# Optimization experiments

Measured on AMD Instinct MI355X. Metric: run time of the kernel, lower is better.

## Reference

```python
import jax, jax.numpy as jnp
import numpy as np

N_HEAD = 16
N_EMBD = 1024
HEAD_DIM = N_EMBD // N_HEAD
ROPE_BASE = 10000.0


def _rope_tables(T, dim):
    inv_freq = 1.0 / (ROPE_BASE ** (jnp.arange(0, dim, 2, dtype=jnp.float32) / dim))
    t = jnp.arange(T, dtype=jnp.float32)
    freqs = jnp.einsum('i,j->ij', t, inv_freq)          # [T, dim/2]
    emb = jnp.concatenate((freqs, freqs), axis=-1)       # [T, dim]
    return jnp.cos(emb), jnp.sin(emb)


def _rotate_half(x):
    x1, x2 = jnp.split(x, 2, axis=-1)
    return jnp.concatenate((-x2, x1), axis=-1)


def setup_inputs() -> dict:
    key = jax.random.key(0)
    k_x, k_wa, k_ba, k_wp, k_bp = jax.random.split(key, 5)
    B, T, C = 2, 2048, N_EMBD
    x = jax.random.normal(k_x, (B, T, C), dtype=jnp.float32)
    # torch Linear weights: [out, in]
    W_attn = jax.random.normal(k_wa, (3 * C, C), dtype=jnp.float32) * (1.0 / np.sqrt(C))
    b_attn = jax.random.normal(k_ba, (3 * C,), dtype=jnp.float32) * 0.01
    W_proj = jax.random.normal(k_wp, (C, C), dtype=jnp.float32) * (1.0 / np.sqrt(C))
    b_proj = jax.random.normal(k_bp, (C,), dtype=jnp.float32) * 0.01
    return {"x": x, "W_attn": W_attn, "b_attn": b_attn, "W_proj": W_proj, "b_proj": b_proj}


def reference(x, W_attn, b_attn, W_proj, b_proj):
    B, T, C = x.shape
    H, D = N_HEAD, HEAD_DIM
    qkv = jnp.einsum('btc,oc->bto', x, W_attn) + b_attn   # [B,T,3C]
    q, k, v = jnp.split(qkv, 3, axis=2)
    # [B,T,C] -> [B,H,T,D]
    q = q.reshape(B, T, H, D).transpose(0, 2, 1, 3)
    k = k.reshape(B, T, H, D).transpose(0, 2, 1, 3)
    v = v.reshape(B, T, H, D).transpose(0, 2, 1, 3)
    cos, sin = _rope_tables(T, D)                          # [T,D]
    q = q * cos + _rotate_half(q) * sin
    k = k * cos + _rotate_half(k) * sin
    att = jnp.einsum('bhqd,bhkd->bhqk', q, k) * (1.0 / np.sqrt(D))
    causal = jnp.tril(jnp.ones((T, T), dtype=bool))
    att = jnp.where(causal, att, -jnp.inf)
    att = jax.nn.softmax(att, axis=-1)
    y = jnp.einsum('bhqk,bhkd->bhqd', att, v)              # [B,H,T,D]
    y = y.transpose(0, 2, 1, 3).reshape(B, T, C)
    y = jnp.einsum('btc,oc->bto', y, W_proj) + b_proj
    return y
```

## Files before the change

### kernel.cpp

```cpp
#include <hip/hip_runtime.h>


typedef unsigned short u16;
typedef u16 u16x4 __attribute__((ext_vector_type(4)));
typedef u16 u16x8 __attribute__((ext_vector_type(8)));
typedef short s16x4 __attribute__((ext_vector_type(4)));
typedef short s16x8 __attribute__((ext_vector_type(8)));
typedef float f32x4 __attribute__((ext_vector_type(4)));

#define T_SEQ 2048
#define C_EMB 1024
#define NH 16
#define HD 64

#define MFMA16(a, b, c) __builtin_amdgcn_mfma_f32_16x16x32_bf16(a, b, c, 0, 0, 0)

__device__ __forceinline__ f32x4 MFMA16K16(s16x4 a, s16x4 b, f32x4 c) {
#if __has_builtin(__builtin_amdgcn_mfma_f32_16x16x16bf16_1k)
    return __builtin_amdgcn_mfma_f32_16x16x16bf16_1k(a, b, c, 0, 0, 0);
#else
    asm("v_mfma_f32_16x16x16_bf16 %0, %1, %2, %0" : "+v"(c) : "v"(a), "v"(b));
    return c;
#endif
}

__device__ __forceinline__ u16 f2bf(float f) {
    union { float f; unsigned int i; } x; x.f = f;
    unsigned int r = x.i + 0x7fffu + ((x.i >> 16) & 1u);
    return (u16)(r >> 16);
}
__device__ __forceinline__ u16x4 pack4(f32x4 v) {
    u16x4 o;
#pragma unroll
    for (int j = 0; j < 4; ++j) o[j] = f2bf(v[j]);
    return o;
}
__device__ __forceinline__ s16x4 pack4cvt_s(f32x4 v) {
    union { s16x4 h; unsigned int w[2]; } u;
    asm("v_cvt_pk_bf16_f32 %0, %1, %2" : "=v"(u.w[0]) : "v"(v[0]), "v"(v[1]));
    asm("v_cvt_pk_bf16_f32 %0, %1, %2" : "=v"(u.w[1]) : "v"(v[2]), "v"(v[3]));
    return u.h;
}
__device__ __forceinline__ void gload16(const void* g, void* l) {
    __builtin_amdgcn_global_load_lds(
        (const __attribute__((address_space(1))) unsigned int*)g,
        (__attribute__((address_space(3))) unsigned int*)l, 16, 0, 0);
}

__global__ __launch_bounds__(256) void prep_k(const float* __restrict__ x, const float* __restrict__ Wa,
                                              const float* __restrict__ Wp,
                                              u16* __restrict__ xb, u16* __restrict__ Wab,
                                              u16* __restrict__ Wpb, float2* __restrict__ tab) {
    int bid = blockIdx.x, tid = threadIdx.x;
    if (bid < 4096) {
        const float* src;
        u16* dst;
        int i;
        if (bid < 2048)      { src = x;  dst = xb;  i = bid * 256 + tid; }
        else if (bid < 3584) { src = Wa; dst = Wab; i = (bid - 2048) * 256 + tid; }
        else                 { src = Wp; dst = Wpb; i = (bid - 3584) * 256 + tid; }
        f32x4 a = ((const f32x4*)src)[i * 2];
        f32x4 b = ((const f32x4*)src)[i * 2 + 1];
        u16x8 o;
#pragma unroll
        for (int j = 0; j < 4; ++j) o[j] = f2bf(a[j]);
#pragma unroll
        for (int j = 0; j < 4; ++j) o[4 + j] = f2bf(b[j]);
        ((u16x8*)dst)[i] = o;
    } else {
        int idx = (bid - 4096) * 256 + tid;
        int t = idx >> 5, j = idx & 31;
        float inv = __builtin_exp2f(-0.41524101186092f * (float)j);
        float s_, c_;
        sincosf((float)t * inv, &s_, &c_);
        tab[idx] = make_float2(c_, s_);
    }
}

__global__ __launch_bounds__(256) void qkv_rope_k(const u16* __restrict__ xb, const u16* __restrict__ Wab,
                                                  const float* __restrict__ bias,
                                                  const float2* __restrict__ tab,
                                                  u16* __restrict__ qb, u16* __restrict__ kb,
                                                  u16* __restrict__ vt) {
    __shared__ u16 smem[24576];
    u16* As = smem;
    u16* Bs = smem + 12288;
    int tid = threadIdx.x;
    int n0 = blockIdx.x * 128, m0 = blockIdx.y * 128;
    int w = tid >> 6, lane = tid & 63, lr = lane & 15, quad = lane >> 4;
    int wr = w >> 1, wc = w & 1;
    f32x4 acc[4][4] = {};
    int srow = tid >> 2;
    int swc8 = (((tid & 3) ^ (srow & 3)) << 3);
    int soff = tid * 8;
    int rc8 = ((quad ^ (lr & 3)) << 3);

#define QKV_STAGE(bufi, kc) do {                                                   \
        int _b = (bufi) * 4096;                                                    \
        gload16(xb  + (size_t)(m0 + srow) * C_EMB + (kc) + swc8,      &As[_b + soff]);        \
        gload16(xb  + (size_t)(m0 + 64 + srow) * C_EMB + (kc) + swc8, &As[_b + 2048 + soff]); \
        gload16(Wab + (size_t)(n0 + srow) * C_EMB + (kc) + swc8,      &Bs[_b + soff]);        \
        gload16(Wab + (size_t)(n0 + 64 + srow) * C_EMB + (kc) + swc8, &Bs[_b + 2048 + soff]); \
    } while (0)

    QKV_STAGE(0, 0);
    QKV_STAGE(1, 32);
    int cur = 0;
    for (int kt = 0; kt < 32; ++kt) {
        if (kt < 30) {
            int nb = cur + 2; if (nb >= 3) nb -= 3;
            QKV_STAGE(nb, (kt + 2) * 32);
            asm volatile("s_waitcnt vmcnt(8)" ::: "memory");
        } else if (kt == 30) {
            asm volatile("s_waitcnt vmcnt(4)" ::: "memory");
        } else {
            asm volatile("s_waitcnt vmcnt(0)" ::: "memory");
        }
        __builtin_amdgcn_s_barrier();
        asm volatile("" ::: "memory");
        int cb = cur * 4096;
        s16x8 af[4], bf[4];
#pragma unroll
        for (int i = 0; i < 4; ++i)
            af[i] = *(const s16x8*)&As[cb + (wr * 64 + i * 16 + lr) * 32 + rc8];
#pragma unroll
        for (int j = 0; j < 4; ++j)
            bf[j] = *(const s16x8*)&Bs[cb + (wc * 64 + j * 16 + lr) * 32 + rc8];
#pragma unroll
        for (int i = 0; i < 4; ++i)
#pragma unroll
            for (int j = 0; j < 4; ++j) acc[i][j] = MFMA16(af[i], bf[j], acc[i][j]);
        asm volatile("" ::: "memory");
        __builtin_amdgcn_s_barrier();
        cur = cur + 1; if (cur >= 3) cur -= 3;
    }
#undef QKV_STAGE

    int sec = n0 >> 10;
    float bv[4];
#pragma unroll
    for (int j = 0; j < 4; ++j) bv[j] = bias[n0 + wc * 64 + j * 16 + lr];

    int h0 = (n0 & 1023) >> 6;
    int b = m0 >> 11, tbase = m0 & 2047;
    if (sec == 2) {
        u16* Ct = smem;
#pragma unroll
        for (int i = 0; i < 4; ++i)
#pragma unroll
            for (int j = 0; j < 4; ++j) {
                f32x4 vv;
#pragma unroll
                for (int r = 0; r < 4; ++r) vv[r] = acc[i][j][r] + bv[j];
                int d = wc * 64 + j * 16 + lr;
                int m4 = wr * 64 + i * 16 + quad * 4;
                *(u16x4*)&Ct[d * 136 + m4] = pack4(vv);
            }
        __syncthreads();
        size_t hb = (size_t)(b * NH);
#pragma unroll
        for (int p = 0; p < 8; ++p) {
            int idx = p * 256 + tid;
            int d = idx >> 4, mc = (idx & 15) << 3;
            s16x8 vdat = *(const s16x8*)&Ct[d * 136 + mc];
            int h = h0 + (d >> 6), dd = d & 63;
            *(s16x8*)(vt + ((hb + h) * HD + dd) * T_SEQ + tbase + mc) = vdat;
        }
    } else {
        u16* dst = (sec == 0) ? qb : kb;
        float qs = (sec == 0) ? 0.18033688011112043f : 1.0f;
        u16* Ct = smem;
        __syncthreads();
#pragma unroll
        for (int i = 0; i < 4; ++i)
#pragma unroll
            for (int r = 0; r < 4; ++r) {
                int mrow = wr * 64 + i * 16 + quad * 4 + r;
                int t = (m0 + mrow) & 2047;
#pragma unroll
                for (int j = 0; j < 2; ++j) {
                    int d1 = j * 16 + lr;
                    float2 cs = tab[t * 32 + d1];
                    float v1 = acc[i][j][r] + bv[j];
                    float v2 = acc[i][j + 2][r] + bv[j + 2];
                    int n1 = wc * 64 + j * 16 + lr;
                    Ct[mrow * 136 + n1]      = f2bf((v1 * cs.x - v2 * cs.y) * qs);
                    Ct[mrow * 136 + n1 + 32] = f2bf((v2 * cs.x + v1 * cs.y) * qs);
                }
            }
        __syncthreads();
#pragma unroll
        for (int p = 0; p < 8; ++p) {
            int idx = p * 256 + tid;
            int mrow = idx >> 4, c = idx & 15;
            s16x8 vdat = *(const s16x8*)&Ct[mrow * 136 + c * 8];
            int h = h0 + (c >> 3), dd = (c & 7) << 3;
            *(s16x8*)(dst + ((size_t)(b * NH + h) * T_SEQ + tbase + mrow) * HD + dd) = vdat;
        }
    }
}

__global__ __launch_bounds__(256, 4) void flash_k(const u16* __restrict__ qb, const u16* __restrict__ kb,
                                                  const u16* __restrict__ vt, u16* __restrict__ yab) {
    __shared__ u16 Ks[2][64 * 72];
    __shared__ u16 Vs[2][64 * 72];
    int tid = threadIdx.x;
    int bx = blockIdx.x, by = blockIdx.y;
    int bh = by;
    int w = tid >> 6, lane = tid & 63, lr = lane & 15, quad = lane >> 4;
    const u16* qh = qb + (size_t)bh * T_SEQ * HD;
    const u16* kh = kb + (size_t)bh * T_SEQ * HD;
    const u16* vh = vt + (size_t)bh * HD * T_SEQ;
    int srow = tid >> 3, sc8 = (tid & 7) << 3;
    int b = bh >> 4, hh = bh & 15;

    for (int ph = 0; ph < 2; ++ph) {
        int qt = ph ? (31 - bx) : bx;
        int q0 = qt * 64;
        int rbase = q0 + w * 16;

        s16x8 aq[2];
#pragma unroll
        for (int ks = 0; ks < 2; ++ks)
            aq[ks] = *(const s16x8*)(qh + (size_t)(rbase + lr) * HD + ks * 32 + quad * 8);

        float m_i = -1e30f;
        f32x4 l4 = {0.f, 0.f, 0.f, 0.f};
        f32x4 oacc[4] = {};

        int ktmax = qt;
        {
            s16x8 ka = *(const s16x8*)(kh + (size_t)srow * HD + sc8);
            s16x8 kb2 = *(const s16x8*)(kh + (size_t)(srow + 32) * HD + sc8);
            s16x8 va = *(const s16x8*)(vh + (size_t)srow * T_SEQ + sc8);
            s16x8 vb = *(const s16x8*)(vh + (size_t)(srow + 32) * T_SEQ + sc8);
            *(s16x8*)&Ks[0][srow * 72 + sc8] = ka;
            *(s16x8*)&Ks[0][(srow + 32) * 72 + sc8] = kb2;
            *(s16x8*)&Vs[0][srow * 72 + sc8] = va;
            *(s16x8*)&Vs[0][(srow + 32) * 72 + sc8] = vb;
        }
        __syncthreads();

        for (int kt = 0; kt <= ktmax; ++kt) {
            int cur = kt & 1;
            int k0 = kt * 64;
            bool pf = kt < ktmax;
            s16x8 kr0, kr1, vr0, vr1;
            if (pf) {
                int kn = k0 + 64;
                kr0 = *(const s16x8*)(kh + (size_t)(kn + srow) * HD + sc8);
                kr1 = *(const s16x8*)(kh + (size_t)(kn + srow + 32) * HD + sc8);
                vr0 = *(const s16x8*)(vh + (size_t)srow * T_SEQ + kn + sc8);
                vr1 = *(const s16x8*)(vh + (size_t)(srow + 32) * T_SEQ + kn + sc8);
            }
            const u16* Kc = Ks[cur];
            const u16* Vc = Vs[cur];

            s16x8 ak[2][4];
#pragma unroll
            for (int ks = 0; ks < 2; ++ks)
#pragma unroll
                for (int tc = 0; tc < 4; ++tc)
                    ak[ks][tc] = *(const s16x8*)&Kc[(tc * 16 + lr) * 72 + ks * 32 + quad * 8];
            s16x4 av[4][4];
#pragma unroll
            for (int dn = 0; dn < 4; ++dn) {
                const u16* vrow = &Vc[(dn * 16 + lr) * 72 + quad * 4];
#pragma unroll
                for (int tc = 0; tc < 4; ++tc)
                    av[dn][tc] = *(const s16x4*)(vrow + tc * 16);
            }
            f32x4 sacc[4] = {};
#pragma unroll
            for (int ks = 0; ks < 2; ++ks)
#pragma unroll
                for (int tc = 0; tc < 4; ++tc) sacc[tc] = MFMA16(ak[ks][tc], aq[ks], sacc[tc]);
            if (kt == ktmax) {
#pragma unroll
                for (int tc = 0; tc < 4; ++tc)
#pragma unroll
                    for (int r = 0; r < 4; ++r)
                        if (k0 + tc * 16 + quad * 4 + r > rbase + lr) sacc[tc][r] = -1e30f;
            }
            f32x4 mv = sacc[0];
#pragma unroll
            for (int tc = 1; tc < 4; ++tc)
#pragma unroll
                for (int r = 0; r < 4; ++r) mv[r] = fmaxf(mv[r], sacc[tc][r]);
            float loc = fmaxf(fmaxf(mv[0], mv[1]), fmaxf(mv[2], mv[3]));
            bool need = !__all(loc <= m_i + 8.0f);
            float alpha = 1.0f;
            if (need) {
                float mx = fmaxf(loc, __shfl_xor(loc, 16, 64));
                mx = fmaxf(mx, __shfl_xor(mx, 32, 64));
                float mn = fmaxf(m_i, mx);
                alpha = __builtin_exp2f(m_i - mn);
                m_i = mn;
#pragma unroll
                for (int r = 0; r < 4; ++r) l4[r] *= alpha;
            }
            float mnow = m_i;
#pragma unroll
            for (int tc = 0; tc < 4; ++tc)
#pragma unroll
                for (int r = 0; r < 4; ++r) {
                    float p = __builtin_exp2f(sacc[tc][r] - mnow);
                    sacc[tc][r] = p;
                    l4[r] += p;
                }
            s16x4 pa[4];
#pragma unroll
            for (int tc = 0; tc < 4; ++tc) pa[tc] = pack4cvt_s(sacc[tc]);
            if (need) {
#pragma unroll
                for (int dn = 0; dn < 4; ++dn)
#pragma unroll
                    for (int r = 0; r < 4; ++r) oacc[dn][r] *= alpha;
            }
#pragma unroll
            for (int dn = 0; dn < 4; ++dn)
#pragma unroll
                for (int tc = 0; tc < 4; ++tc)
                    oacc[dn] = MFMA16K16(av[dn][tc], pa[tc], oacc[dn]);

            if (pf) {
                int nx = cur ^ 1;
                *(s16x8*)&Ks[nx][srow * 72 + sc8] = kr0;
                *(s16x8*)&Ks[nx][(srow + 32) * 72 + sc8] = kr1;
                *(s16x8*)&Vs[nx][srow * 72 + sc8] = vr0;
                *(s16x8*)&Vs[nx][(srow + 32) * 72 + sc8] = vr1;
            }
            __syncthreads();
        }
        float rs = (l4[0] + l4[1]) + (l4[2] + l4[3]);
        rs += __shfl_xor(rs, 16, 64);
        rs += __shfl_xor(rs, 32, 64);
        {
            float inv = 1.f / rs;
            int t = rbase + lr;
            size_t base = ((size_t)b * T_SEQ + t) * C_EMB + hh * HD;
#pragma unroll
            for (int dn = 0; dn < 4; ++dn) {
                f32x4 vv;
#pragma unroll
                for (int r = 0; r < 4; ++r) vv[r] = oacc[dn][r] * inv;
                *(u16x4*)(yab + base + dn * 16 + quad * 4) = pack4(vv);
            }
        }
    }
}

__global__ __launch_bounds__(256) void proj_k(const u16* __restrict__ ya, const u16* __restrict__ Wpb,
                                              const float* __restrict__ bias, float* __restrict__ out) {
    __shared__ u16 As[2][2048];
    __shared__ u16 Bs[2][2048];
    int tid = threadIdx.x;
    int n0 = blockIdx.x * 64, m0 = blockIdx.y * 64;
    int w = tid >> 6, lane = tid & 63, lr = lane & 15, quad = lane >> 4;
    int wr = w >> 1, wc = w & 1;
    f32x4 acc[2][2] = {};
    int srow = tid >> 2;
    int swc8 = (((tid & 3) ^ (srow & 3)) << 3);
    int soff = tid * 8;
    int rc8 = ((quad ^ (lr & 3)) << 3);

#define PRJ_STAGE(bufi, kc) do {                                                   \
        gload16(ya  + (size_t)(m0 + srow) * C_EMB + (kc) + swc8, &As[bufi][soff]); \
        gload16(Wpb + (size_t)(n0 + srow) * C_EMB + (kc) + swc8, &Bs[bufi][soff]); \
    } while (0)

    PRJ_STAGE(0, 0);
#pragma unroll 2
    for (int kt = 0; kt < 32; ++kt) {
        int cur = kt & 1;
        if (kt < 31) {
            PRJ_STAGE(cur ^ 1, (kt + 1) * 32);
            asm volatile("s_waitcnt vmcnt(2)" ::: "memory");
        } else {
            asm volatile("s_waitcnt vmcnt(0)" ::: "memory");
        }
        __builtin_amdgcn_s_barrier();
        asm volatile("" ::: "memory");
        s16x8 af[2], bf[2];
#pragma unroll
        for (int i = 0; i < 2; ++i)
            af[i] = *(const s16x8*)&As[cur][(wr * 32 + i * 16 + lr) * 32 + rc8];
#pragma unroll
        for (int j = 0; j < 2; ++j)
            bf[j] = *(const s16x8*)&Bs[cur][(wc * 32 + j * 16 + lr) * 32 + rc8];
#pragma unroll
        for (int i = 0; i < 2; ++i)
#pragma unroll
            for (int j = 0; j < 2; ++j) acc[i][j] = MFMA16(af[i], bf[j], acc[i][j]);
        asm volatile("" ::: "memory");
        __builtin_amdgcn_s_barrier();
    }
#undef PRJ_STAGE

    float bv[2];
#pragma unroll
    for (int j = 0; j < 2; ++j) bv[j] = bias[n0 + wc * 32 + j * 16 + lr];
#pragma unroll
    for (int i = 0; i < 2; ++i)
#pragma unroll
        for (int r = 0; r < 4; ++r) {
            int m = m0 + wr * 32 + i * 16 + quad * 4 + r;
#pragma unroll
            for (int j = 0; j < 2; ++j)
                out[(size_t)m * C_EMB + n0 + wc * 32 + j * 16 + lr] = acc[i][j][r] + bv[j];
        }
}

extern "C" void kernel_launch(void* const* d_in, const int* in_sizes, int n_in,
                              void* d_out, int out_size, void* d_ws, size_t ws_size,
                              hipStream_t stream) {
    const float *x = nullptr, *Wa = nullptr, *ba = nullptr, *Wp = nullptr, *bp = nullptr;
    for (int i = 0; i < n_in; ++i) {
        switch (in_sizes[i]) {
            case 4194304: x  = (const float*)d_in[i]; break;
            case 3145728: Wa = (const float*)d_in[i]; break;
            case 3072:    ba = (const float*)d_in[i]; break;
            case 1048576: Wp = (const float*)d_in[i]; break;
            case 1024:    bp = (const float*)d_in[i]; break;
            default: break;
        }
    }
    float* out = (float*)d_out;

    char* ws = (char*)d_ws;
    u16* qb     = (u16*)(ws);
    u16* kb     = (u16*)(ws + 8388608);
    u16* vt     = (u16*)(ws + 16777216);
    u16* yab    = (u16*)(ws + 25165824);
    float2* tab = (float2*)(ws + 33554432);
    u16* xb     = (u16*)(ws + 35651584);
    u16* Wab    = (u16*)(ws + 44040192);
    u16* Wpb    = (u16*)(ws + 50331648);

    prep_k<<<4352, 256, 0, stream>>>(x, Wa, Wp, xb, Wab, Wpb, tab);
    qkv_rope_k<<<dim3(24, 32), 256, 0, stream>>>(xb, Wab, ba, tab, qb, kb, vt);
    flash_k<<<dim3(16, 32), 256, 0, stream>>>(qb, kb, vt, yab);
    proj_k<<<dim3(16, 64), 256, 0, stream>>>(yab, Wpb, bp, out);
}
```

Baseline: 197.8 us.

## Share K/V tiles across both paired query strips in one flash pass

The flash kernel used to process its two causal-balanced query tiles (bx and 31-bx) one after another, reloading the K/V tiles from global memory for each. It now keeps both query strips' accumulators live and walks the K/V sequence once, applying each staged tile to both strips. This roughly halves K/V global loads and LDS staging, and removes the second prologue and its sync. The cost is a doubled register footprint for accumulators and softmax state, so launch bounds drop from 4 to 2 blocks per SM, which may reduce occupancy and latency hiding.

```diff
diff --git a/kernel.cpp b/kernel.cpp
--- a/kernel.cpp
+++ b/kernel.cpp
@@ -200,13 +200,12 @@
     }
 }
 
-__global__ __launch_bounds__(256, 4) void flash_k(const u16* __restrict__ qb, const u16* __restrict__ kb,
+__global__ __launch_bounds__(256, 2) void flash_k(const u16* __restrict__ qb, const u16* __restrict__ kb,
                                                   const u16* __restrict__ vt, u16* __restrict__ yab) {
     __shared__ u16 Ks[2][64 * 72];
     __shared__ u16 Vs[2][64 * 72];
     int tid = threadIdx.x;
-    int bx = blockIdx.x, by = blockIdx.y;
-    int bh = by;
+    int bx = blockIdx.x, bh = blockIdx.y;
     int w = tid >> 6, lane = tid & 63, lr = lane & 15, quad = lane >> 4;
     const u16* qh = qb + (size_t)bh * T_SEQ * HD;
     const u16* kh = kb + (size_t)bh * T_SEQ * HD;
@@ -214,138 +213,149 @@
     int srow = tid >> 3, sc8 = (tid & 7) << 3;
     int b = bh >> 4, hh = bh & 15;
 
+    int qtA = bx, qtB = 31 - bx;
+    int rbA = qtA * 64 + w * 16, rbB = qtB * 64 + w * 16;
+
+    s16x8 aqA[2], aqB[2];
+#pragma unroll
+    for (int ks = 0; ks < 2; ++ks) {
+        aqA[ks] = *(const s16x8*)(qh + (size_t)(rbA + lr) * HD + ks * 32 + quad * 8);
+        aqB[ks] = *(const s16x8*)(qh + (size_t)(rbB + lr) * HD + ks * 32 + quad * 8);
+    }
+
+    float mA = -1e30f, mB = -1e30f;
+    f32x4 lA = {0.f, 0.f, 0.f, 0.f}, lB = {0.f, 0.f, 0.f, 0.f};
+    f32x4 oA[4] = {}, oB[4] = {};
+
+#define DO_STRIP(AQ, MI, L4, OACC, QT, RBASE) do {                                  \
+        f32x4 sacc[4] = {};                                                         \
+_Pragma("unroll")                                                                   \
+        for (int ks = 0; ks < 2; ++ks)                                              \
+_Pragma("unroll")                                                                   \
+            for (int tc = 0; tc < 4; ++tc) sacc[tc] = MFMA16(ak[ks][tc], AQ[ks], sacc[tc]); \
+        if (kt == (QT)) {                                                           \
+_Pragma("unroll")                                                                   \
+            for (int tc = 0; tc < 4; ++tc)                                          \
+_Pragma("unroll")                                                                   \
+                for (int r = 0; r < 4; ++r)                                         \
+                    if (k0 + tc * 16 + quad * 4 + r > (RBASE) + lr) sacc[tc][r] = -1e30f; \
+        }                                                                           \
+        f32x4 mv = sacc[0];                                                         \
+_Pragma("unroll")                                                                   \
+        for (int tc = 1; tc < 4; ++tc)                                              \
+_Pragma("unroll")                                                                   \
+            for (int r = 0; r < 4; ++r) mv[r] = fmaxf(mv[r], sacc[tc][r]);          \
+        float loc = fmaxf(fmaxf(mv[0], mv[1]), fmaxf(mv[2], mv[3]));                \
+        bool need = !__all(loc <= (MI) + 8.0f);                                     \
+        float alpha = 1.0f;                                                         \
+        if (need) {                                                                 \
+            float mx = fmaxf(loc, __shfl_xor(loc, 16, 64));                         \
+            mx = fmaxf(mx, __shfl_xor(mx, 32, 64));                                 \
+            float mn = fmaxf((MI), mx);                                             \
+            alpha = __builtin_exp2f((MI) - mn);                                     \
+            (MI) = mn;                                                              \
+_Pragma("unroll")                                                                   \
+            for (int r = 0; r < 4; ++r) (L4)[r] *= alpha;                           \
+        }                                                                           \
+        float mnow = (MI);                                                          \
+_Pragma("unroll")                                                                   \
+        for (int tc = 0; tc < 4; ++tc)                                              \
+_Pragma("unroll")                                                                   \
+            for (int r = 0; r < 4; ++r) {                                           \
+                float p = __builtin_exp2f(sacc[tc][r] - mnow);                      \
+                sacc[tc][r] = p;                                                    \
+                (L4)[r] += p;                                                       \
+            }                                                                       \
+        s16x4 pa[4];                                                                \
+_Pragma("unroll")                                                                   \
+        for (int tc = 0; tc < 4; ++tc) pa[tc] = pack4cvt_s(sacc[tc]);               \
+        if (need) {                                                                 \
+_Pragma("unroll")                                                                   \
+            for (int dn = 0; dn < 4; ++dn)                                          \
+_Pragma("unroll")                                                                   \
+                for (int r = 0; r < 4; ++r) (OACC)[dn][r] *= alpha;                 \
+        }                                                                           \
+_Pragma("unroll")                                                                   \
+        for (int dn = 0; dn < 4; ++dn)                                              \
+_Pragma("unroll")                                                                   \
+            for (int tc = 0; tc < 4; ++tc)                                          \
+                (OACC)[dn] = MFMA16K16(av[dn][tc], pa[tc], (OACC)[dn]);             \
+    } while (0)
+
+    int ktmax = qtB;
+    {
+        s16x8 ka = *(const s16x8*)(kh + (size_t)srow * HD + sc8);
+        s16x8 kb2 = *(const s16x8*)(kh + (size_t)(srow + 32) * HD + sc8);
+        s16x8 va = *(const s16x8*)(vh + (size_t)srow * T_SEQ + sc8);
+        s16x8 vb = *(const s16x8*)(vh + (size_t)(srow + 32) * T_SEQ + sc8);
+        *(s16x8*)&Ks[0][srow * 72 + sc8] = ka;
+        *(s16x8*)&Ks[0][(srow + 32) * 72 + sc8] = kb2;
+        *(s16x8*)&Vs[0][srow * 72 + sc8] = va;
+        *(s16x8*)&Vs[0][(srow + 32) * 72 + sc8] = vb;
+    }
+    __syncthreads();
+
+    for (int kt = 0; kt <= ktmax; ++kt) {
+        int cur = kt & 1;
+        int k0 = kt * 64;
+        bool pf = kt < ktmax;
+        s16x8 kr0, kr1, vr0, vr1;
+        if (pf) {
+            int kn = k0 + 64;
+            kr0 = *(const s16x8*)(kh + (size_t)(kn + srow) * HD + sc8);
+            kr1 = *(const s16x8*)(kh + (size_t)(kn + srow + 32) * HD + sc8);
+            vr0 = *(const s16x8*)(vh + (size_t)srow * T_SEQ + kn + sc8);
+            vr1 = *(const s16x8*)(vh + (size_t)(srow + 32) * T_SEQ + kn + sc8);
+        }
+        const u16* Kc = Ks[cur];
+        const u16* Vc = Vs[cur];
+
+        s16x8 ak[2][4];
+#pragma unroll
+        for (int ks = 0; ks < 2; ++ks)
+#pragma unroll
+            for (int tc = 0; tc < 4; ++tc)
+                ak[ks][tc] = *(const s16x8*)&Kc[(tc * 16 + lr) * 72 + ks * 32 + quad * 8];
+        s16x4 av[4][4];
+#pragma unroll
+        for (int dn = 0; dn < 4; ++dn) {
+            const u16* vrow = &Vc[(dn * 16 + lr) * 72 + quad * 4];
+#pragma unroll
+            for (int tc = 0; tc < 4; ++tc)
+                av[dn][tc] = *(const s16x4*)(vrow + tc * 16);
+        }
+
+        if (kt <= qtA) DO_STRIP(aqA, mA, lA, oA, qtA, rbA);
+        DO_STRIP(aqB, mB, lB, oB, qtB, rbB);
+
+        if (pf) {
+            int nx = cur ^ 1;
+            *(s16x8*)&Ks[nx][srow * 72 + sc8] = kr0;
+            *(s16x8*)&Ks[nx][(srow + 32) * 72 + sc8] = kr1;
+            *(s16x8*)&Vs[nx][srow * 72 + sc8] = vr0;
+            *(s16x8*)&Vs[nx][(srow + 32) * 72 + sc8] = vr1;
+        }
+        __syncthreads();
+    }
+#undef DO_STRIP
+
+#pragma unroll
     for (int ph = 0; ph < 2; ++ph) {
-        int qt = ph ? (31 - bx) : bx;
-        int q0 = qt * 64;
-        int rbase = q0 + w * 16;
-
-        s16x8 aq[2];
-#pragma unroll
-        for (int ks = 0; ks < 2; ++ks)
-            aq[ks] = *(const s16x8*)(qh + (size_t)(rbase + lr) * HD + ks * 32 + quad * 8);
-
-        float m_i = -1e30f;
-        f32x4 l4 = {0.f, 0.f, 0.f, 0.f};
-        f32x4 oacc[4] = {};
-
-        int ktmax = qt;
-        {
-            s16x8 ka = *(const s16x8*)(kh + (size_t)srow * HD + sc8);
-            s16x8 kb2 = *(const s16x8*)(kh + (size_t)(srow + 32) * HD + sc8);
-            s16x8 va = *(const s16x8*)(vh + (size_t)srow * T_SEQ + sc8);
-            s16x8 vb = *(const s16x8*)(vh + (size_t)(srow + 32) * T_SEQ + sc8);
-            *(s16x8*)&Ks[0][srow * 72 + sc8] = ka;
-            *(s16x8*)&Ks[0][(srow + 32) * 72 + sc8] = kb2;
-            *(s16x8*)&Vs[0][srow * 72 + sc8] = va;
-            *(s16x8*)&Vs[0][(srow + 32) * 72 + sc8] = vb;
-        }
-        __syncthreads();
-
-        for (int kt = 0; kt <= ktmax; ++kt) {
-            int cur = kt & 1;
-            int k0 = kt * 64;
-            bool pf = kt < ktmax;
-            s16x8 kr0, kr1, vr0, vr1;
-            if (pf) {
-                int kn = k0 + 64;
-                kr0 = *(const s16x8*)(kh + (size_t)(kn + srow) * HD + sc8);
-                kr1 = *(const s16x8*)(kh + (size_t)(kn + srow + 32) * HD + sc8);
-                vr0 = *(const s16x8*)(vh + (size_t)srow * T_SEQ + kn + sc8);
-                vr1 = *(const s16x8*)(vh + (size_t)(srow + 32) * T_SEQ + kn + sc8);
-            }
-            const u16* Kc = Ks[cur];
-            const u16* Vc = Vs[cur];
-
-            s16x8 ak[2][4];
-#pragma unroll
-            for (int ks = 0; ks < 2; ++ks)
-#pragma unroll
-                for (int tc = 0; tc < 4; ++tc)
-                    ak[ks][tc] = *(const s16x8*)&Kc[(tc * 16 + lr) * 72 + ks * 32 + quad * 8];
-            s16x4 av[4][4];
-#pragma unroll
-            for (int dn = 0; dn < 4; ++dn) {
-                const u16* vrow = &Vc[(dn * 16 + lr) * 72 + quad * 4];
-#pragma unroll
-                for (int tc = 0; tc < 4; ++tc)
-                    av[dn][tc] = *(const s16x4*)(vrow + tc * 16);
-            }
-            f32x4 sacc[4] = {};
-#pragma unroll
-            for (int ks = 0; ks < 2; ++ks)
-#pragma unroll
-                for (int tc = 0; tc < 4; ++tc) sacc[tc] = MFMA16(ak[ks][tc], aq[ks], sacc[tc]);
-            if (kt == ktmax) {
-#pragma unroll
-                for (int tc = 0; tc < 4; ++tc)
-#pragma unroll
-                    for (int r = 0; r < 4; ++r)
-                        if (k0 + tc * 16 + quad * 4 + r > rbase + lr) sacc[tc][r] = -1e30f;
-            }
-            f32x4 mv = sacc[0];
-#pragma unroll
-            for (int tc = 1; tc < 4; ++tc)
-#pragma unroll
-                for (int r = 0; r < 4; ++r) mv[r] = fmaxf(mv[r], sacc[tc][r]);
-            float loc = fmaxf(fmaxf(mv[0], mv[1]), fmaxf(mv[2], mv[3]));
-            bool need = !__all(loc <= m_i + 8.0f);
-            float alpha = 1.0f;
-            if (need) {
-                float mx = fmaxf(loc, __shfl_xor(loc, 16, 64));
-                mx = fmaxf(mx, __shfl_xor(mx, 32, 64));
-                float mn = fmaxf(m_i, mx);
-                alpha = __builtin_exp2f(m_i - mn);
-                m_i = mn;
-#pragma unroll
-                for (int r = 0; r < 4; ++r) l4[r] *= alpha;
-            }
-            float mnow = m_i;
-#pragma unroll
-            for (int tc = 0; tc < 4; ++tc)
-#pragma unroll
-                for (int r = 0; r < 4; ++r) {
-                    float p = __builtin_exp2f(sacc[tc][r] - mnow);
-                    sacc[tc][r] = p;
-                    l4[r] += p;
-                }
-            s16x4 pa[4];
-#pragma unroll
-            for (int tc = 0; tc < 4; ++tc) pa[tc] = pack4cvt_s(sacc[tc]);
-            if (need) {
-#pragma unroll
-                for (int dn = 0; dn < 4; ++dn)
-#pragma unroll
-                    for (int r = 0; r < 4; ++r) oacc[dn][r] *= alpha;
-            }
-#pragma unroll
-            for (int dn = 0; dn < 4; ++dn)
-#pragma unroll
-                for (int tc = 0; tc < 4; ++tc)
-                    oacc[dn] = MFMA16K16(av[dn][tc], pa[tc], oacc[dn]);
-
-            if (pf) {
-                int nx = cur ^ 1;
-                *(s16x8*)&Ks[nx][srow * 72 + sc8] = kr0;
-                *(s16x8*)&Ks[nx][(srow + 32) * 72 + sc8] = kr1;
-                *(s16x8*)&Vs[nx][srow * 72 + sc8] = vr0;
-                *(s16x8*)&Vs[nx][(srow + 32) * 72 + sc8] = vr1;
-            }
-            __syncthreads();
-        }
+        f32x4* oacc = ph ? oB : oA;
+        f32x4& l4 = ph ? lB : lA;
+        int rbase = ph ? rbB : rbA;
         float rs = (l4[0] + l4[1]) + (l4[2] + l4[3]);
         rs += __shfl_xor(rs, 16, 64);
         rs += __shfl_xor(rs, 32, 64);
-        {
-            float inv = 1.f / rs;
-            int t = rbase + lr;
-            size_t base = ((size_t)b * T_SEQ + t) * C_EMB + hh * HD;
-#pragma unroll
-            for (int dn = 0; dn < 4; ++dn) {
-                f32x4 vv;
-#pragma unroll
-                for (int r = 0; r < 4; ++r) vv[r] = oacc[dn][r] * inv;
-                *(u16x4*)(yab + base + dn * 16 + quad * 4) = pack4(vv);
-            }
+        float inv = 1.f / rs;
+        int t = rbase + lr;
+        size_t base = ((size_t)b * T_SEQ + t) * C_EMB + hh * HD;
+#pragma unroll
+        for (int dn = 0; dn < 4; ++dn) {
+            f32x4 vv;
+#pragma unroll
+            for (int r = 0; r < 4; ++r) vv[r] = oacc[dn][r] * inv;
+            *(u16x4*)(yab + base + dn * 16 + quad * 4) = pack4(vv);
         }
     }
 }
```

Measured after the change: 195.3 us. About the same (-1.2%).
